# Kernel optimization log

Hardware: AMD Instinct MI355X
Metric: run time of the kernel (lower is better)

## Reference

```python
import jax, jax.numpy as jnp
import numpy as np

NEG_SLOPE = 0.2

def setup_inputs() -> dict:
    key = jax.random.key(0)
    k1, k2, k3 = jax.random.split(key, 3)
    x = jax.random.normal(k1, (4, 4096, 64), dtype=jnp.float32)
    weight_key = jax.random.normal(k2, (64, 1), dtype=jnp.float32)
    weight_query = jax.random.normal(k3, (64, 1), dtype=jnp.float32)
    return {"x": x, "weight_key": weight_key, "weight_query": weight_query}

def reference(x, weight_key, weight_query):
    # x: [bz, N, F]; key/query: [bz, N, 1]
    k = jnp.matmul(x, weight_key)          # [bz, N, 1]
    q = jnp.matmul(x, weight_query)        # [bz, N, 1]
    # additive broadcast attention: scores[b,i,j] = k[b,i] + q[b,j]
    scores = k + jnp.swapaxes(q, 1, 2)     # [bz, N, N]
    scores = jax.nn.leaky_relu(scores, negative_slope=NEG_SLOPE)
    attention = jax.nn.softmax(scores, axis=2)
    # dropout is identity in eval mode
    attn_feat = jnp.matmul(attention, x)   # [bz, N, F]
    return jnp.transpose(attn_feat, (0, 2, 1))  # [bz, F, N]
```

## Files before the change

### kernel.cpp

```cpp
#include <hip/hip_runtime.h>

#define N 4096
#define F 64
#define BZ 4
#define MAGIC1 0x1F2E3D4Cu
#define MAGIC2 0x5A6B7C8Du

__device__ __forceinline__ unsigned int f2ord(float f) {
    unsigned int u = __float_as_uint(f);
    return (u & 0x80000000u) ? ~u : (u ^ 0x80000000u);
}
__device__ __forceinline__ float ord2f(unsigned int v) {
    unsigned int b = (v & 0x80000000u) ? (v ^ 0x80000000u) : ~v;
    return __uint_as_float(b);
}

__device__ __forceinline__ void batch_barrier(unsigned* bflags, unsigned magic,
                                              int cid, int tid, int wave, int lane) {
    __syncthreads();
    if (tid == 0) {
        __builtin_amdgcn_fence(__ATOMIC_RELEASE, "agent");
        __hip_atomic_store(bflags + cid, magic, __ATOMIC_RELAXED,
                           __HIP_MEMORY_SCOPE_AGENT);
    }
    if (wave == 0) {
        for (;;) {
            unsigned a = __hip_atomic_load(bflags + lane, __ATOMIC_RELAXED,
                                           __HIP_MEMORY_SCOPE_AGENT);
            if (__all(a == magic)) break;
            __builtin_amdgcn_s_sleep(4);
        }
        __builtin_amdgcn_fence(__ATOMIC_ACQUIRE, "agent");
    }
    __syncthreads();
    asm volatile("" ::: "memory");
}

__global__ __launch_bounds__(1024) void fused_gat(
        const float* __restrict__ x, const float* __restrict__ wk,
        const float* __restrict__ wq, unsigned* __restrict__ flags1,
        unsigned* __restrict__ flags2, float* __restrict__ karr,
        unsigned long long* __restrict__ qkey, float* __restrict__ q_sorted,
        unsigned int* __restrict__ ordidx, int* __restrict__ pA,
        float* __restrict__ out) {
    __shared__ __align__(16) char smem[66176];
    const int bid = blockIdx.x;
    const int tid = threadIdx.x;
    const int wave = tid >> 6, lane = tid & 63;
    const int b = bid >> 6, chunk = bid & 63;
    unsigned* bf1 = flags1 + (b << 6);
    unsigned* bf2 = flags2 + (b << 6);

    float* kks = (float*)(smem + 36864);

    if (tid == 0)
        __hip_atomic_store(bf2 + chunk, 0u, __ATOMIC_RELAXED,
                           __HIP_MEMORY_SCOPE_AGENT);

    {
        const int row = tid >> 4;
        const int fq = tid & 15;
        const int grow = (chunk << 6) + row;
        const int f0 = fq << 2;
        float4 xv = *(const float4*)(x + ((size_t)b * N + grow) * F + f0);
        float4 k4 = *(const float4*)(wk + f0);
        float4 q4 = *(const float4*)(wq + f0);
        float kk = xv.x * k4.x + xv.y * k4.y + xv.z * k4.z + xv.w * k4.w;
        float qq = xv.x * q4.x + xv.y * q4.y + xv.z * q4.z + xv.w * q4.w;
#pragma unroll
        for (int off = 1; off <= 8; off <<= 1) {
            kk += __shfl_xor(kk, off, 16);
            qq += __shfl_xor(qq, off, 16);
        }
        if (fq == 0) {
            kks[row] = kk;
            karr[b * N + grow] = kk;
            qkey[b * N + grow] = ((unsigned long long)f2ord(qq) << 32)
                               | (unsigned int)grow;
        }
    }
    batch_barrier(bf1, MAGIC1, chunk, tid, wave, lane);

    {
        unsigned long long* qs = (unsigned long long*)smem;
        unsigned short (*pc)[64] = (unsigned short(*)[64])(smem + 32768);
        unsigned short (*pc2)[64] = (unsigned short(*)[64])(smem + 34816);
        const unsigned long long* qb = qkey + b * N;
        for (int t = tid; t < N; t += 1024) qs[t] = qb[t];
        const float kk = kks[lane];
        const unsigned int thetaOrd = f2ord(-kk);
        __syncthreads();

        const unsigned long long myKey = qs[(chunk << 6) + lane];
        int cnt = 0, cnt2 = 0;
        const ulonglong2* q2 = (const ulonglong2*)qs;
        const int s0 = wave * 128;
#pragma unroll 8
        for (int t2 = 0; t2 < 128; ++t2) {
            ulonglong2 v = q2[s0 + t2];
            cnt  += (int)(v.x < myKey) + (int)(v.y < myKey);
            cnt2 += (int)((unsigned int)(v.x >> 32) < thetaOrd)
                  + (int)((unsigned int)(v.y >> 32) < thetaOrd);
        }
        pc[wave][lane]  = (unsigned short)cnt;
        pc2[wave][lane] = (unsigned short)cnt2;
        __syncthreads();

        if (wave == 0) {
            int r = 0, p = 0;
#pragma unroll
            for (int w = 0; w < 16; ++w) { r += pc[w][lane]; p += pc2[w][lane]; }
            q_sorted[b * N + r] = ord2f((unsigned int)(myKey >> 32));
            ordidx[b * N + r] = (unsigned int)(myKey & 0xFFFFFFFFu);
            pA[b * N + (chunk << 6) + lane] = p;
        }
    }
    batch_barrier(bf2, MAGIC2, chunk, tid, wave, lane);

    {
        const int f = chunk;
        float* SUF1 = (float*)smem;
        float* PRE2 = (float*)(smem + 16416);
        float* SUFD = (float*)(smem + 32832);
        float* PRED = (float*)(smem + 49248);
        float* wt1  = (float*)(smem + 65664);
        float* wtd1 = (float*)(smem + 65728);
        float* wt2  = (float*)(smem + 65792);
        float* wtd2 = (float*)(smem + 65856);
        float* wb1  = (float*)(smem + 65920);
        float* wbd1 = (float*)(smem + 65984);
        float* wb2  = (float*)(smem + 66048);
        float* wbd2 = (float*)(smem + 66112);
        const int t0 = tid << 2;
        const float* qsb = q_sorted + b * N;
        const float Qmax = qsb[N - 1];

        float4 qv = *(const float4*)(qsb + t0);
        uint4 iv = *(const uint4*)(ordidx + b * N + t0);
        float qa[4] = {qv.x, qv.y, qv.z, qv.w};
        unsigned ia[4] = {iv.x & (N - 1), iv.y & (N - 1),
                          iv.z & (N - 1), iv.w & (N - 1)};
        float e1[4], e2[4], w1[4], w2[4];
        const float* xbf = x + (size_t)b * N * F + f;
#pragma unroll
        for (int r = 0; r < 4; ++r) {
            float d = qa[r] - Qmax;
            e1[r] = __expf(d);
            e2[r] = __expf(0.2f * d);
            float xf = xbf[(size_t)ia[r] * F];
            w1[r] = e1[r] * xf;
            w2[r] = e2[r] * xf;
        }

        float lp2_0 = 0.f, lp2_1 = w2[0], lp2_2 = lp2_1 + w2[1], lp2_3 = lp2_2 + w2[2];
        float T2 = lp2_3 + w2[3];
        float lpd_0 = 0.f, lpd_1 = e2[0], lpd_2 = lpd_1 + e2[1], lpd_3 = lpd_2 + e2[2];
        float TD2 = lpd_3 + e2[3];
        float ls1_3 = w1[3], ls1_2 = w1[2] + ls1_3, ls1_1 = w1[1] + ls1_2, ls1_0 = w1[0] + ls1_1;
        float T1 = ls1_0;
        float lsd_3 = e1[3], lsd_2 = e1[2] + lsd_3, lsd_1 = e1[1] + lsd_2, lsd_0 = e1[0] + lsd_1;
        float TD1 = lsd_0;

        float ip2 = T2, ipd2 = TD2;
#pragma unroll
        for (int d = 1; d < 64; d <<= 1) {
            float n1 = __shfl_up(ip2, d, 64);
            float n2 = __shfl_up(ipd2, d, 64);
            if (lane >= d) { ip2 += n1; ipd2 += n2; }
        }
        float is1 = T1, isd1 = TD1;
#pragma unroll
        for (int d = 1; d < 64; d <<= 1) {
            float n1 = __shfl_down(is1, d, 64);
            float n2 = __shfl_down(isd1, d, 64);
            if (lane + d < 64) { is1 += n1; isd1 += n2; }
        }
        if (lane == 63) { wt2[wave] = ip2; wtd2[wave] = ipd2; }
        if (lane == 0)  { wt1[wave] = is1; wtd1[wave] = isd1; }
        __syncthreads();
        if (wave == 0 && lane < 16) {
            float v = wt2[lane], vd = wtd2[lane];
            float s = v, sd = vd;
#pragma unroll
            for (int d = 1; d < 16; d <<= 1) {
                float n1 = __shfl_up(s, d, 64);
                float n2 = __shfl_up(sd, d, 64);
                if (lane >= d) { s += n1; sd += n2; }
            }
            wb2[lane] = s - v; wbd2[lane] = sd - vd;
            if (lane == 15) { PRE2[N] = s; PRED[N] = sd; }
        }
        if (wave == 1 && lane < 16) {
            float v = wt1[lane], vd = wtd1[lane];
            float s = v, sd = vd;
#pragma unroll
            for (int d = 1; d < 16; d <<= 1) {
                float n1 = __shfl_down(s, d, 64);
                float n2 = __shfl_down(sd, d, 64);
                if (lane + d < 16) { s += n1; sd += n2; }
            }
            wb1[lane] = s - v; wbd1[lane] = sd - vd;
            if (lane == 0) { SUF1[N] = 0.f; SUFD[N] = 0.f; }
        }
        __syncthreads();
        float bp2 = wb2[wave] + (ip2 - T2);
        float bpd = wbd2[wave] + (ipd2 - TD2);
        float bs1 = wb1[wave] + (is1 - T1);
        float bsd = wbd1[wave] + (isd1 - TD1);
        float4 o;
        o.x = bp2 + lp2_0; o.y = bp2 + lp2_1; o.z = bp2 + lp2_2; o.w = bp2 + lp2_3;
        *(float4*)(PRE2 + t0) = o;
        o.x = bpd + lpd_0; o.y = bpd + lpd_1; o.z = bpd + lpd_2; o.w = bpd + lpd_3;
        *(float4*)(PRED + t0) = o;
        o.x = bs1 + ls1_0; o.y = bs1 + ls1_1; o.z = bs1 + ls1_2; o.w = bs1 + ls1_3;
        *(float4*)(SUF1 + t0) = o;
        o.x = bsd + lsd_0; o.y = bsd + lsd_1; o.z = bsd + lsd_2; o.w = bsd + lsd_3;
        *(float4*)(SUFD + t0) = o;
        __syncthreads();

        float4 kv = *(const float4*)(karr + b * N + t0);
        int4 pv = *(const int4*)(pA + b * N + t0);
        float ka[4] = {kv.x, kv.y, kv.z, kv.w};
        int pa[4] = {pv.x, pv.y, pv.z, pv.w};
        float ra[4];
#pragma unroll
        for (int r = 0; r < 4; ++r) {
            float kk = ka[r];
            int p = pa[r];
            if ((unsigned)p > N) p = N;
            float u = kk + Qmax;
            float M = fmaxf(u, 0.2f * u);
            float c1 = __expf(u - M);
            float c2 = __expf(0.2f * u - M);
            float num = c1 * SUF1[p] + c2 * PRE2[p];
            float den = c1 * SUFD[p] + c2 * PRED[p];
            ra[r] = num / den;
        }
        float4 res; res.x = ra[0]; res.y = ra[1]; res.z = ra[2]; res.w = ra[3];
        *(float4*)(out + ((size_t)(b * F + f)) * N + t0) = res;
    }

    if (tid == 0)
        __hip_atomic_store(bf1 + chunk, 0u, __ATOMIC_RELAXED,
                           __HIP_MEMORY_SCOPE_AGENT);
}

extern "C" void kernel_launch(void* const* d_in, const int* in_sizes, int n_in,
                              void* d_out, int out_size, void* d_ws, size_t ws_size,
                              hipStream_t stream) {
    const float* x  = (const float*)d_in[0];
    const float* wk = (const float*)d_in[1];
    const float* wq = (const float*)d_in[2];
    float* out = (float*)d_out;

    float* wsf = (float*)d_ws;
    unsigned* flags1 = (unsigned*)wsf;
    unsigned* flags2 = flags1 + 256;
    float* karr = wsf + 512;
    unsigned long long* qkey = (unsigned long long*)(wsf + 512 + BZ * N);
    float* q_sorted = wsf + 512 + 3 * BZ * N;
    unsigned int* ordidx = (unsigned int*)(wsf + 512 + 4 * BZ * N);
    int* pA = (int*)(wsf + 512 + 5 * BZ * N);

    fused_gat<<<BZ * 64, 1024, 0, stream>>>(x, wk, wq, flags1, flags2, karr,
                                            qkey, q_sorted, ordidx, pA, out);
}
```

Before: 96.20 us.

## Replace barrier fences with relaxed atomics and pack workspace data into 64-bit words

```diff
diff --git a/kernel.cpp b/kernel.cpp
--- a/kernel.cpp
+++ b/kernel.cpp
@@ -6,6 +6,9 @@
 #define MAGIC1 0x1F2E3D4Cu
 #define MAGIC2 0x5A6B7C8Du
 
+#define ALOAD(p)     __hip_atomic_load((p),  __ATOMIC_RELAXED, __HIP_MEMORY_SCOPE_AGENT)
+#define ASTORE(p, v) __hip_atomic_store((p), (v), __ATOMIC_RELAXED, __HIP_MEMORY_SCOPE_AGENT)
+
 __device__ __forceinline__ unsigned int f2ord(float f) {
     unsigned int u = __float_as_uint(f);
     return (u & 0x80000000u) ? ~u : (u ^ 0x80000000u);
@@ -18,19 +21,13 @@
 __device__ __forceinline__ void batch_barrier(unsigned* bflags, unsigned magic,
                                               int cid, int tid, int wave, int lane) {
     __syncthreads();
-    if (tid == 0) {
-        __builtin_amdgcn_fence(__ATOMIC_RELEASE, "agent");
-        __hip_atomic_store(bflags + cid, magic, __ATOMIC_RELAXED,
-                           __HIP_MEMORY_SCOPE_AGENT);
-    }
+    if (tid == 0) ASTORE(bflags + cid, magic);
     if (wave == 0) {
         for (;;) {
-            unsigned a = __hip_atomic_load(bflags + lane, __ATOMIC_RELAXED,
-                                           __HIP_MEMORY_SCOPE_AGENT);
+            unsigned a = ALOAD(bflags + lane);
             if (__all(a == magic)) break;
-            __builtin_amdgcn_s_sleep(4);
-        }
-        __builtin_amdgcn_fence(__ATOMIC_ACQUIRE, "agent");
+            __builtin_amdgcn_s_sleep(2);
+        }
     }
     __syncthreads();
     asm volatile("" ::: "memory");
@@ -39,11 +36,12 @@
 __global__ __launch_bounds__(1024) void fused_gat(
         const float* __restrict__ x, const float* __restrict__ wk,
         const float* __restrict__ wq, unsigned* __restrict__ flags1,
-        unsigned* __restrict__ flags2, float* __restrict__ karr,
-        unsigned long long* __restrict__ qkey, float* __restrict__ q_sorted,
-        unsigned int* __restrict__ ordidx, int* __restrict__ pA,
+        unsigned* __restrict__ flags2,
+        unsigned long long* __restrict__ qkey,
+        unsigned long long* __restrict__ skey,
+        unsigned long long* __restrict__ kp,
         float* __restrict__ out) {
-    __shared__ __align__(16) char smem[66176];
+    __shared__ __align__(16) char smem[66432];
     const int bid = blockIdx.x;
     const int tid = threadIdx.x;
     const int wave = tid >> 6, lane = tid & 63;
@@ -53,9 +51,7 @@
 
     float* kks = (float*)(smem + 36864);
 
-    if (tid == 0)
-        __hip_atomic_store(bf2 + chunk, 0u, __ATOMIC_RELAXED,
-                           __HIP_MEMORY_SCOPE_AGENT);
+    if (tid == 0) ASTORE(bf2 + chunk, 0u);
 
     {
         const int row = tid >> 4;
@@ -74,9 +70,8 @@
         }
         if (fq == 0) {
             kks[row] = kk;
-            karr[b * N + grow] = kk;
-            qkey[b * N + grow] = ((unsigned long long)f2ord(qq) << 32)
-                               | (unsigned int)grow;
+            ASTORE(qkey + b * N + grow,
+                   ((unsigned long long)f2ord(qq) << 32) | (unsigned int)grow);
         }
     }
     batch_barrier(bf1, MAGIC1, chunk, tid, wave, lane);
@@ -86,7 +81,7 @@
         unsigned short (*pc)[64] = (unsigned short(*)[64])(smem + 32768);
         unsigned short (*pc2)[64] = (unsigned short(*)[64])(smem + 34816);
         const unsigned long long* qb = qkey + b * N;
-        for (int t = tid; t < N; t += 1024) qs[t] = qb[t];
+        for (int t = tid; t < N; t += 1024) qs[t] = ALOAD(qb + t);
         const float kk = kks[lane];
         const unsigned int thetaOrd = f2ord(-kk);
         __syncthreads();
@@ -110,15 +105,16 @@
             int r = 0, p = 0;
 #pragma unroll
             for (int w = 0; w < 16; ++w) { r += pc[w][lane]; p += pc2[w][lane]; }
-            q_sorted[b * N + r] = ord2f((unsigned int)(myKey >> 32));
-            ordidx[b * N + r] = (unsigned int)(myKey & 0xFFFFFFFFu);
-            pA[b * N + (chunk << 6) + lane] = p;
+            ASTORE(skey + b * N + r, myKey);
+            ASTORE(kp + b * N + (chunk << 6) + lane,
+                   ((unsigned long long)__float_as_uint(kk) << 32)
+                 | (unsigned int)p);
         }
     }
     batch_barrier(bf2, MAGIC2, chunk, tid, wave, lane);
 
     {
-        const int f = chunk;
+        const int f = ((chunk & 7) << 3) | (chunk >> 3);
         float* SUF1 = (float*)smem;
         float* PRE2 = (float*)(smem + 16416);
         float* SUFD = (float*)(smem + 32832);
@@ -131,23 +127,30 @@
         float* wbd1 = (float*)(smem + 65984);
         float* wb2  = (float*)(smem + 66048);
         float* wbd2 = (float*)(smem + 66112);
+        float* QmaxS = (float*)(smem + 66176);
         const int t0 = tid << 2;
-        const float* qsb = q_sorted + b * N;
-        const float Qmax = qsb[N - 1];
-
-        float4 qv = *(const float4*)(qsb + t0);
-        uint4 iv = *(const uint4*)(ordidx + b * N + t0);
-        float qa[4] = {qv.x, qv.y, qv.z, qv.w};
-        unsigned ia[4] = {iv.x & (N - 1), iv.y & (N - 1),
-                          iv.z & (N - 1), iv.w & (N - 1)};
+
+        if (tid == 0)
+            QmaxS[0] = ord2f((unsigned int)(ALOAD(skey + b * N + N - 1) >> 32));
+        __syncthreads();
+        const float Qmax = QmaxS[0];
+
+        unsigned long long sk[4], kv[4];
+#pragma unroll
+        for (int r = 0; r < 4; ++r) {
+            sk[r] = ALOAD(skey + b * N + t0 + r);
+            kv[r] = ALOAD(kp + b * N + t0 + r);
+        }
         float e1[4], e2[4], w1[4], w2[4];
         const float* xbf = x + (size_t)b * N * F + f;
 #pragma unroll
         for (int r = 0; r < 4; ++r) {
-            float d = qa[r] - Qmax;
+            float qv = ord2f((unsigned int)(sk[r] >> 32));
+            unsigned ia = (unsigned int)sk[r] & (N - 1);
+            float d = qv - Qmax;
             e1[r] = __expf(d);
             e2[r] = __expf(0.2f * d);
-            float xf = xbf[(size_t)ia[r] * F];
+            float xf = xbf[(size_t)ia * F];
             w1[r] = e1[r] * xf;
             w2[r] = e2[r] * xf;
         }
@@ -218,15 +221,11 @@
         *(float4*)(SUFD + t0) = o;
         __syncthreads();
 
-        float4 kv = *(const float4*)(karr + b * N + t0);
-        int4 pv = *(const int4*)(pA + b * N + t0);
-        float ka[4] = {kv.x, kv.y, kv.z, kv.w};
-        int pa[4] = {pv.x, pv.y, pv.z, pv.w};
         float ra[4];
 #pragma unroll
         for (int r = 0; r < 4; ++r) {
-            float kk = ka[r];
-            int p = pa[r];
+            float kk = __uint_as_float((unsigned int)(kv[r] >> 32));
+            int p = (int)(kv[r] & 0xFFFFFFFFu);
             if ((unsigned)p > N) p = N;
             float u = kk + Qmax;
             float M = fmaxf(u, 0.2f * u);
@@ -240,9 +239,7 @@
         *(float4*)(out + ((size_t)(b * F + f)) * N + t0) = res;
     }
 
-    if (tid == 0)
-        __hip_atomic_store(bf1 + chunk, 0u, __ATOMIC_RELAXED,
-                           __HIP_MEMORY_SCOPE_AGENT);
+    if (tid == 0) ASTORE(bf1 + chunk, 0u);
 }
 
 extern "C" void kernel_launch(void* const* d_in, const int* in_sizes, int n_in,
@@ -256,12 +253,10 @@
     float* wsf = (float*)d_ws;
     unsigned* flags1 = (unsigned*)wsf;
     unsigned* flags2 = flags1 + 256;
-    float* karr = wsf + 512;
-    unsigned long long* qkey = (unsigned long long*)(wsf + 512 + BZ * N);
-    float* q_sorted = wsf + 512 + 3 * BZ * N;
-    unsigned int* ordidx = (unsigned int*)(wsf + 512 + 4 * BZ * N);
-    int* pA = (int*)(wsf + 512 + 5 * BZ * N);
-
-    fused_gat<<<BZ * 64, 1024, 0, stream>>>(x, wk, wq, flags1, flags2, karr,
-                                            qkey, q_sorted, ordidx, pA, out);
-}
+    unsigned long long* qkey = (unsigned long long*)(wsf + 512);
+    unsigned long long* skey = qkey + BZ * N;
+    unsigned long long* kp   = skey + BZ * N;
+
+    fused_gat<<<BZ * 64, 1024, 0, stream>>>(x, wk, wq, flags1, flags2,
+                                            qkey, skey, kp, out);
+}
```

Result: faster. 83.54 us (-13.2%).
